# Performance work log

Measured on AMD Instinct MI355X. Metric: run time of the kernel, lower is better.

Reference implementation:

```python
import jax, jax.numpy as jnp
import numpy as np

NUM_TAG = 1024
TAG_DIM = 128
COMMITMENT_COST = 0.25
B, W = 128, 1024


def setup_inputs() -> dict:
    key = jax.random.key(0)
    k1, k2 = jax.random.split(key)
    inputs = jax.random.normal(k1, (B, W, TAG_DIM), dtype=jnp.float32)
    # torch init: uniform_(-1/num_tag, 1/num_tag)
    codebook = jax.random.uniform(k2, (NUM_TAG, TAG_DIM), dtype=jnp.float32,
                                  minval=-1.0 / NUM_TAG, maxval=1.0 / NUM_TAG)
    return {"inputs": inputs, "codebook": codebook}


def reference(inputs, codebook):
    # inputs: [B, W, D], codebook: [K, D]
    D = inputs.shape[-1]
    flat = inputs.reshape(-1, D)  # [N, D]
    distances = (jnp.sum(flat * flat, axis=1, keepdims=True)
                 + jnp.sum(codebook * codebook, axis=1)
                 - 2.0 * flat @ codebook.T)
    encoding_indices = jnp.argmin(distances, axis=1)  # [N]
    quantized = codebook[encoding_indices].reshape(inputs.shape)  # [B, W, D]
    e_latent_loss = jnp.mean((jax.lax.stop_gradient(quantized) - inputs) ** 2)
    q_latent_loss = jnp.mean((quantized - jax.lax.stop_gradient(inputs)) ** 2)
    vq_loss = q_latent_loss + COMMITMENT_COST * e_latent_loss
    # straight-through estimator
    quantized_st = inputs + jax.lax.stop_gradient(quantized - inputs)
    return (quantized_st, vq_loss, encoding_indices.reshape(inputs.shape[:-1]))
```

## Files before the change

kernel.cpp:

```cpp
#include <hip/hip_runtime.h>

#define NUM_TAG 1024
#define TAG_DIM 128
#define NROWS   131072
#define FLAG_M  1.25e-4f
#define RPG     8
#define RF      4

typedef __attribute__((ext_vector_type(8))) short short8;
typedef __attribute__((ext_vector_type(4))) float f32x4;

__device__ inline void split2(float xv, unsigned short& h, unsigned short& m) {
    unsigned xb = __float_as_uint(xv);
    unsigned hb = xb & 0xFFFF0000u;
    float r1 = xv - __uint_as_float(hb);
    unsigned mb = __float_as_uint(r1) & 0xFFFF0000u;
    h = (unsigned short)(hb >> 16);
    m = (unsigned short)(mb >> 16);
}

__device__ inline void gld_lds16(const void* g, void* l) {
    __builtin_amdgcn_global_load_lds(
        (const __attribute__((address_space(1))) void*)g,
        (__attribute__((address_space(3))) void*)l, 16, 0, 0);
}

__global__ __launch_bounds__(256) void prep_kernel(
    const float* __restrict__ cb, float* __restrict__ scc,
    unsigned short* __restrict__ cbf, int* __restrict__ count)
{
    int t = blockIdx.x * 256 + threadIdx.x;
    if (t == 0) count[0] = 0;
    {
        int l  = t & 63;
        int s  = (t >> 6) & 3;
        int ch = t >> 8;
        int k  = ch * 16 + (l & 15);
        int d0 = s * 32 + (l >> 4) * 8;
        const float4* xp = reinterpret_cast<const float4*>(cb) + k * 32 + (d0 >> 2);
        float4 v0 = xp[0], v1 = xp[1];
        float xv[8] = {v0.x, v0.y, v0.z, v0.w, v1.x, v1.y, v1.z, v1.w};
        short8 hh, mm;
#pragma unroll
        for (int e = 0; e < 8; ++e) {
            unsigned short h, m;
            split2(xv[e], h, m);
            hh[e] = (short)h; mm[e] = (short)m;
        }
        long baseh = (long)ch * 4096 + (((0 * 4) + s) * 64 + l) * 8;
        long basem = (long)ch * 4096 + (((1 * 4) + s) * 64 + l) * 8;
        *reinterpret_cast<short8*>(cbf + baseh) = hh;
        *reinterpret_cast<short8*>(cbf + basem) = mm;
    }
    if (t < NUM_TAG) {
        const float4* row = reinterpret_cast<const float4*>(cb) + t * (TAG_DIM / 4);
        float s = 0.f;
#pragma unroll
        for (int i = 0; i < TAG_DIM / 4; ++i) {
            float4 v = row[i];
            s += v.x * v.x; s += v.y * v.y; s += v.z * v.z; s += v.w * v.w;
        }
        scc[t] = s;
    }
}

__global__ __launch_bounds__(64, 2) void argmin_mfma_kernel(
    const float* __restrict__ x,
    const unsigned short* __restrict__ cbf,
    const float* __restrict__ scc,
    float* __restrict__ fidx_out,
    int* __restrict__ list, int* __restrict__ count)
{
    __shared__ __align__(16) unsigned short lds[2][4096];
    __shared__ float scc_lds[NUM_TAG];

    const int l   = threadIdx.x & 63;
    const int l15 = l & 15;
    const int l4  = l >> 4;
    const int row0 = blockIdx.x * 64;

    const float4* gsrc = reinterpret_cast<const float4*>(cbf);

#pragma unroll
    for (int i = 0; i < 4; ++i)
        gld_lds16(reinterpret_cast<const float4*>(scc) + i * 64 + l,
                  (void*)(scc_lds + (i * 64 + l) * 4));
#pragma unroll
    for (int i = 0; i < 8; ++i)
        gld_lds16(gsrc + i * 64 + l, (void*)&lds[0][(i * 64 + l) * 8]);
#pragma unroll
    for (int i = 0; i < 8; ++i)
        gld_lds16(gsrc + 512 + i * 64 + l, (void*)&lds[1][(i * 64 + l) * 8]);

    short8 Ah[RF][4], Am[RF][4];
#pragma unroll
    for (int rf = 0; rf < RF; ++rf) {
        const float4* xp = reinterpret_cast<const float4*>(x) +
                           (long)(row0 + rf * 16 + l15) * 32 + l4 * 2;
#pragma unroll
        for (int s = 0; s < 4; ++s) {
            float4 v0 = xp[s * 8];
            float4 v1 = xp[s * 8 + 1];
            float xv[8] = {v0.x, v0.y, v0.z, v0.w, v1.x, v1.y, v1.z, v1.w};
#pragma unroll
            for (int e = 0; e < 8; ++e) {
                unsigned short h, m;
                split2(xv[e], h, m);
                Ah[rf][s][e] = (short)h;
                Am[rf][s][e] = (short)m;
            }
        }
    }

    float m1[RF][4], m2[RF][4]; int i1[RF][4];
#pragma unroll
    for (int rf = 0; rf < RF; ++rf)
#pragma unroll
        for (int r = 0; r < 4; ++r) { m1[rf][r] = 3.4e38f; m2[rf][r] = 3.4e38f; i1[rf][r] = 0; }

    for (int ch = 0; ch < 64; ++ch) {
        const int b = ch & 1;
        if (ch < 63) { asm volatile("s_waitcnt vmcnt(8)" ::: "memory"); }
        else         { asm volatile("s_waitcnt vmcnt(0)" ::: "memory"); }
        __builtin_amdgcn_sched_barrier(0);

        short8 Bh[4], Bm[4];
#pragma unroll
        for (int s = 0; s < 4; ++s) {
            Bh[s] = *reinterpret_cast<const short8*>(&lds[b][(((0 * 4) + s) * 64 + l) * 8]);
            Bm[s] = *reinterpret_cast<const short8*>(&lds[b][(((1 * 4) + s) * 64 + l) * 8]);
        }
        const float sccv = scc_lds[ch * 16 + l15];

        asm volatile("s_waitcnt lgkmcnt(0)" ::: "memory");
        __builtin_amdgcn_sched_barrier(0);

        if (ch + 2 < 64) {
            const float4* gp = gsrc + (ch + 2) * 512 + l;
#pragma unroll
            for (int i = 0; i < 8; ++i)
                gld_lds16(gp + i * 64, (void*)&lds[b][(i * 64 + l) * 8]);
        }

        f32x4 acc[RF];
#pragma unroll
        for (int rf = 0; rf < RF; ++rf) acc[rf] = (f32x4)0.f;

#pragma unroll
        for (int s = 0; s < 4; ++s)
#pragma unroll
            for (int rf = 0; rf < RF; ++rf) {
                acc[rf] = __builtin_amdgcn_mfma_f32_16x16x32_bf16(Ah[rf][s], Bm[s], acc[rf], 0, 0, 0);
                acc[rf] = __builtin_amdgcn_mfma_f32_16x16x32_bf16(Am[rf][s], Bh[s], acc[rf], 0, 0, 0);
                acc[rf] = __builtin_amdgcn_mfma_f32_16x16x32_bf16(Ah[rf][s], Bh[s], acc[rf], 0, 0, 0);
            }

        const int k = ch * 16 + l15;
#pragma unroll
        for (int rf = 0; rf < RF; ++rf)
#pragma unroll
            for (int r = 0; r < 4; ++r) {
                float score = sccv - 2.0f * acc[rf][r];
                m2[rf][r] = __builtin_amdgcn_fmed3f(score, m1[rf][r], m2[rf][r]);
                i1[rf][r] = (score < m1[rf][r]) ? k : i1[rf][r];
                m1[rf][r] = fminf(m1[rf][r], score);
            }
    }

#pragma unroll
    for (int rf = 0; rf < RF; ++rf)
#pragma unroll
        for (int r = 0; r < 4; ++r) {
            float v1 = m1[rf][r], v2 = m2[rf][r]; int ii = i1[rf][r];
#pragma unroll
            for (int mk = 1; mk < 16; mk <<= 1) {
                float o1 = __shfl_xor(v1, mk, 64);
                float o2 = __shfl_xor(v2, mk, 64);
                int   oi = __shfl_xor(ii, mk, 64);
                float n2 = fminf(fminf(v2, o2), fmaxf(v1, o1));
                if (o1 < v1 || (o1 == v1 && oi < ii)) { v1 = o1; ii = oi; }
                v2 = n2;
            }
            if (l15 == 0) {
                int row = row0 + rf * 16 + l4 * 4 + r;
                fidx_out[row] = (float)ii;
                if (v2 - v1 <= FLAG_M) {
                    int pos = atomicAdd(count, 1);
                    list[pos] = row;
                }
            }
        }
}

__global__ __launch_bounds__(256) void exact_fix_kernel(
    const float* __restrict__ x, const float* __restrict__ cb,
    const float* __restrict__ scc, const int* __restrict__ list,
    const int* __restrict__ count, float* __restrict__ fidx_out)
{
    __shared__ float4 Xs[RPG][32];
    __shared__ float  sxxs[RPG];
    __shared__ float  wrv[RPG][4];
    __shared__ int    wri[RPG][4];
    __shared__ int    rows_s[RPG];

    const int tid  = threadIdx.x;
    const int lane = tid & 63;
    const int wv   = tid >> 6;
    const int nflag = count[0];
    const int ngroups = (nflag + RPG - 1) / RPG;

    for (int g = blockIdx.x; g < ngroups; g += gridDim.x) {
        const int nr = min(RPG, nflag - g * RPG);
        if (tid < RPG)
            rows_s[tid] = list[g * RPG + min(tid, nr - 1)];
        __syncthreads();
        {
            int r = tid >> 5, i = tid & 31;
            Xs[r][i] = reinterpret_cast<const float4*>(x)[(long)rows_s[r] * 32 + i];
        }
        __syncthreads();
        if (tid < RPG) {
            float s = 0.f;
            for (int i = 0; i < 32; ++i) {
                float4 v = Xs[tid][i];
                s += v.x * v.x; s += v.y * v.y; s += v.z * v.z; s += v.w * v.w;
            }
            sxxs[tid] = s;
        }
        __syncthreads();

        float acc[RPG][4];
#pragma unroll
        for (int r = 0; r < RPG; ++r)
#pragma unroll
            for (int j = 0; j < 4; ++j) acc[r][j] = 0.f;

        const float4* crow = reinterpret_cast<const float4*>(cb) + (tid * 4) * 32;
        for (int i = 0; i < 32; ++i) {
            float4 xv[RPG];
#pragma unroll
            for (int r = 0; r < RPG; ++r) xv[r] = Xs[r][i];
#pragma unroll
            for (int j = 0; j < 4; ++j) {
                float4 c = crow[j * 32 + i];
#pragma unroll
                for (int r = 0; r < RPG; ++r) {
                    acc[r][j] += xv[r].x * c.x;
                    acc[r][j] += xv[r].y * c.y;
                    acc[r][j] += xv[r].z * c.z;
                    acc[r][j] += xv[r].w * c.w;
                }
            }
        }

#pragma unroll
        for (int r = 0; r < RPG; ++r) {
            float bv = 3.4e38f; int bi = 0;
            const float sxxv = sxxs[r];
#pragma unroll
            for (int j = 0; j < 4; ++j) {
                int k = tid * 4 + j;
                float s1 = sxxv + scc[k];
                float dist = s1 - 2.0f * acc[r][j];
                if (dist < bv) { bv = dist; bi = k; }
            }
#pragma unroll
            for (int mk = 1; mk < 64; mk <<= 1) {
                float ov = __shfl_xor(bv, mk, 64);
                int   oi = __shfl_xor(bi, mk, 64);
                if (ov < bv || (ov == bv && oi < bi)) { bv = ov; bi = oi; }
            }
            if (lane == 0) { wrv[r][wv] = bv; wri[r][wv] = bi; }
        }
        __syncthreads();
        if (tid < RPG && tid < nr) {
            float bv = wrv[tid][0]; int bi = wri[tid][0];
#pragma unroll
            for (int e = 1; e < 4; ++e) {
                float v = wrv[tid][e]; int oi = wri[tid][e];
                if (v < bv || (v == bv && oi < bi)) { bv = v; bi = oi; }
            }
            fidx_out[rows_s[tid]] = (float)bi;
        }
        __syncthreads();
    }
}

__global__ __launch_bounds__(256) void quant_kernel(
    const float* __restrict__ x, const float* __restrict__ cb,
    const float* __restrict__ fidx, float* __restrict__ out,
    double* __restrict__ partial)
{
    const int N4 = NROWS * (TAG_DIM / 4);
    double s = 0.0;
    for (int i = blockIdx.x * blockDim.x + threadIdx.x; i < N4; i += gridDim.x * blockDim.x) {
        int n = i >> 5;
        int d4 = i & 31;
        int k = (int)fidx[n];
        float4 xv = reinterpret_cast<const float4*>(x)[i];
        float4 qv = reinterpret_cast<const float4*>(cb)[k * 32 + d4];
        float dx = qv.x - xv.x, dy = qv.y - xv.y, dz = qv.z - xv.z, dw = qv.w - xv.w;
        float4 o;
        o.x = xv.x + dx; o.y = xv.y + dy; o.z = xv.z + dz; o.w = xv.w + dw;
        reinterpret_cast<float4*>(out)[i] = o;
        s += (double)dx * dx; s += (double)dy * dy; s += (double)dz * dz; s += (double)dw * dw;
    }
    __shared__ double sd[256];
    sd[threadIdx.x] = s;
    __syncthreads();
    for (int off = 128; off > 0; off >>= 1) {
        if (threadIdx.x < (unsigned)off) sd[threadIdx.x] += sd[threadIdx.x + off];
        __syncthreads();
    }
    if (threadIdx.x == 0) partial[blockIdx.x] = sd[0];
}

__global__ __launch_bounds__(256) void loss_kernel(
    const double* __restrict__ partial, int n, float* __restrict__ out_loss)
{
    __shared__ double sd[256];
    double s = 0.0;
    for (int i = threadIdx.x; i < n; i += 256) s += partial[i];
    sd[threadIdx.x] = s;
    __syncthreads();
    for (int off = 128; off > 0; off >>= 1) {
        if (threadIdx.x < (unsigned)off) sd[threadIdx.x] += sd[threadIdx.x + off];
        __syncthreads();
    }
    if (threadIdx.x == 0) {
        double mean = sd[0] / (double)((long long)NROWS * TAG_DIM);
        out_loss[0] = (float)(mean + 0.25 * mean);
    }
}

extern "C" void kernel_launch(void* const* d_in, const int* in_sizes, int n_in,
                              void* d_out, int out_size, void* d_ws, size_t ws_size,
                              hipStream_t stream) {
    const float* x  = (const float*)d_in[0];
    const float* cb = (const float*)d_in[1];
    float* out      = (float*)d_out;
    float* out_loss = out + (long)NROWS * TAG_DIM;
    float* out_fidx = out_loss + 1;

    char* wsb = (char*)d_ws;
    float*          scc     = (float*)(wsb);
    unsigned short* cbf     = (unsigned short*)(wsb + 4096);
    int*            list    = (int*)(wsb + 528384);
    int*            count   = (int*)(wsb + 1052672);
    double*         partial = (double*)(wsb + 1052736);

    prep_kernel       <<<64, 256, 0, stream>>>(cb, scc, cbf, count);
    argmin_mfma_kernel<<<NROWS / 64, 64, 0, stream>>>(x, cbf, scc, out_fidx, list, count);
    exact_fix_kernel  <<<512, 256, 0, stream>>>(x, cb, scc, list, count, out_fidx);
    quant_kernel      <<<2048, 256, 0, stream>>>(x, cb, out_fidx, out, partial);
    loss_kernel       <<<1, 256, 0, stream>>>(partial, 2048, out_loss);
}
```

Baseline: 249.1 us.

## Split argmin block across two waves sharing codebook LDS staging

The argmin kernel now runs two wavefronts per block, each handling 32 rows (RF 2) instead of one wave handling 64 rows. The codebook chunk loads into LDS are split between the waves, and block barriers are added around the double-buffered LDS reads and refills. The aim is lower per-wave register pressure, higher occupancy and cooperative loading. In exchange it adds two s_barrier calls per chunk and halves MFMA reuse of each B fragment per wave.

```diff
diff --git a/kernel.cpp b/kernel.cpp
--- a/kernel.cpp
+++ b/kernel.cpp
@@ -5,7 +5,7 @@
 #define NROWS   131072
 #define FLAG_M  1.25e-4f
 #define RPG     8
-#define RF      4
+#define RF      2
 
 typedef __attribute__((ext_vector_type(8))) short short8;
 typedef __attribute__((ext_vector_type(4))) float f32x4;
@@ -64,7 +64,7 @@
     }
 }
 
-__global__ __launch_bounds__(64, 2) void argmin_mfma_kernel(
+__global__ __launch_bounds__(128, 3) void argmin_mfma_kernel(
     const float* __restrict__ x,
     const unsigned short* __restrict__ cbf,
     const float* __restrict__ scc,
@@ -74,23 +74,31 @@
     __shared__ __align__(16) unsigned short lds[2][4096];
     __shared__ float scc_lds[NUM_TAG];
 
-    const int l   = threadIdx.x & 63;
+    const int tid = threadIdx.x;
+    const int w   = tid >> 6;
+    const int l   = tid & 63;
     const int l15 = l & 15;
     const int l4  = l >> 4;
-    const int row0 = blockIdx.x * 64;
+    const int row0 = blockIdx.x * 64 + w * 32;
 
     const float4* gsrc = reinterpret_cast<const float4*>(cbf);
 
 #pragma unroll
-    for (int i = 0; i < 4; ++i)
-        gld_lds16(reinterpret_cast<const float4*>(scc) + i * 64 + l,
-                  (void*)(scc_lds + (i * 64 + l) * 4));
-#pragma unroll
-    for (int i = 0; i < 8; ++i)
-        gld_lds16(gsrc + i * 64 + l, (void*)&lds[0][(i * 64 + l) * 8]);
-#pragma unroll
-    for (int i = 0; i < 8; ++i)
-        gld_lds16(gsrc + 512 + i * 64 + l, (void*)&lds[1][(i * 64 + l) * 8]);
+    for (int i = 0; i < 2; ++i) {
+        int idx = i * 128 + w * 64 + l;
+        gld_lds16(reinterpret_cast<const float4*>(scc) + idx,
+                  (void*)(scc_lds + idx * 4));
+    }
+#pragma unroll
+    for (int i = 0; i < 4; ++i) {
+        int j = w * 4 + i;
+        gld_lds16(gsrc + j * 64 + l, (void*)&lds[0][(j * 64 + l) * 8]);
+    }
+#pragma unroll
+    for (int i = 0; i < 4; ++i) {
+        int j = w * 4 + i;
+        gld_lds16(gsrc + 512 + j * 64 + l, (void*)&lds[1][(j * 64 + l) * 8]);
+    }
 
     short8 Ah[RF][4], Am[RF][4];
 #pragma unroll
@@ -120,8 +128,9 @@
 
     for (int ch = 0; ch < 64; ++ch) {
         const int b = ch & 1;
-        if (ch < 63) { asm volatile("s_waitcnt vmcnt(8)" ::: "memory"); }
+        if (ch < 63) { asm volatile("s_waitcnt vmcnt(4)" ::: "memory"); }
         else         { asm volatile("s_waitcnt vmcnt(0)" ::: "memory"); }
+        __builtin_amdgcn_s_barrier();
         __builtin_amdgcn_sched_barrier(0);
 
         short8 Bh[4], Bm[4];
@@ -134,12 +143,15 @@
 
         asm volatile("s_waitcnt lgkmcnt(0)" ::: "memory");
         __builtin_amdgcn_sched_barrier(0);
+        __builtin_amdgcn_s_barrier();
 
         if (ch + 2 < 64) {
             const float4* gp = gsrc + (ch + 2) * 512 + l;
 #pragma unroll
-            for (int i = 0; i < 8; ++i)
-                gld_lds16(gp + i * 64, (void*)&lds[b][(i * 64 + l) * 8]);
+            for (int i = 0; i < 4; ++i) {
+                int j = w * 4 + i;
+                gld_lds16(gp + j * 64, (void*)&lds[b][(j * 64 + l) * 8]);
+            }
         }
 
         f32x4 acc[RF];
@@ -350,7 +362,7 @@
     double*         partial = (double*)(wsb + 1052736);
 
     prep_kernel       <<<64, 256, 0, stream>>>(cb, scc, cbf, count);
-    argmin_mfma_kernel<<<NROWS / 64, 64, 0, stream>>>(x, cbf, scc, out_fidx, list, count);
+    argmin_mfma_kernel<<<NROWS / 64, 128, 0, stream>>>(x, cbf, scc, out_fidx, list, count);
     exact_fix_kernel  <<<512, 256, 0, stream>>>(x, cb, scc, list, count, out_fidx);
     quant_kernel      <<<2048, 256, 0, stream>>>(x, cb, out_fidx, out, partial);
     loss_kernel       <<<1, 256, 0, stream>>>(partial, 2048, out_loss);
```

Result: no change. 248.6 us (-0.2%).

## Drop codebook low-bf16 split, read codebook from global, shrink row tile

Applied to the files above, without the earlier changes.

The codebook is now stored as a single bf16 high part, so each k-chunk needs two MFMAs per row fragment instead of three. The flagging margin is widened and the exact-fix kernel gets more blocks to absorb the extra near-ties. The LDS double-buffer fed by global_load_lds is replaced by direct register loads from global memory, with a two-stage software prefetch. Rows per block drop from 64 to 32 with a higher occupancy hint. This trades fewer MFMAs and less LDS use for more approximate scores and more rows sent to the exact fallback path, plus repeated global reads of the codebook.

```diff
diff --git a/kernel.cpp b/kernel.cpp
--- a/kernel.cpp
+++ b/kernel.cpp
@@ -3,9 +3,9 @@
 #define NUM_TAG 1024
 #define TAG_DIM 128
 #define NROWS   131072
-#define FLAG_M  1.25e-4f
+#define FLAG_M  5.5e-4f
 #define RPG     8
-#define RF      4
+#define RF      2
 
 typedef __attribute__((ext_vector_type(8))) short short8;
 typedef __attribute__((ext_vector_type(4))) float f32x4;
@@ -17,12 +17,6 @@
     unsigned mb = __float_as_uint(r1) & 0xFFFF0000u;
     h = (unsigned short)(hb >> 16);
     m = (unsigned short)(mb >> 16);
-}
-
-__device__ inline void gld_lds16(const void* g, void* l) {
-    __builtin_amdgcn_global_load_lds(
-        (const __attribute__((address_space(1))) void*)g,
-        (__attribute__((address_space(3))) void*)l, 16, 0, 0);
 }
 
 __global__ __launch_bounds__(256) void prep_kernel(
@@ -40,17 +34,11 @@
         const float4* xp = reinterpret_cast<const float4*>(cb) + k * 32 + (d0 >> 2);
         float4 v0 = xp[0], v1 = xp[1];
         float xv[8] = {v0.x, v0.y, v0.z, v0.w, v1.x, v1.y, v1.z, v1.w};
-        short8 hh, mm;
-#pragma unroll
-        for (int e = 0; e < 8; ++e) {
-            unsigned short h, m;
-            split2(xv[e], h, m);
-            hh[e] = (short)h; mm[e] = (short)m;
-        }
-        long baseh = (long)ch * 4096 + (((0 * 4) + s) * 64 + l) * 8;
-        long basem = (long)ch * 4096 + (((1 * 4) + s) * 64 + l) * 8;
-        *reinterpret_cast<short8*>(cbf + baseh) = hh;
-        *reinterpret_cast<short8*>(cbf + basem) = mm;
+        short8 hh;
+#pragma unroll
+        for (int e = 0; e < 8; ++e)
+            hh[e] = (short)(unsigned short)(__float_as_uint(xv[e]) >> 16);
+        *reinterpret_cast<short8*>(cbf + (long)ch * 2048 + ((s * 64 + l) * 8)) = hh;
     }
     if (t < NUM_TAG) {
         const float4* row = reinterpret_cast<const float4*>(cb) + t * (TAG_DIM / 4);
@@ -64,33 +52,24 @@
     }
 }
 
-__global__ __launch_bounds__(64, 2) void argmin_mfma_kernel(
+__global__ __launch_bounds__(64, 3) void argmin_mfma_kernel(
     const float* __restrict__ x,
     const unsigned short* __restrict__ cbf,
     const float* __restrict__ scc,
     float* __restrict__ fidx_out,
     int* __restrict__ list, int* __restrict__ count)
 {
-    __shared__ __align__(16) unsigned short lds[2][4096];
     __shared__ float scc_lds[NUM_TAG];
 
     const int l   = threadIdx.x & 63;
     const int l15 = l & 15;
     const int l4  = l >> 4;
-    const int row0 = blockIdx.x * 64;
-
-    const float4* gsrc = reinterpret_cast<const float4*>(cbf);
+    const int row0 = blockIdx.x * 32;
 
 #pragma unroll
     for (int i = 0; i < 4; ++i)
-        gld_lds16(reinterpret_cast<const float4*>(scc) + i * 64 + l,
-                  (void*)(scc_lds + (i * 64 + l) * 4));
-#pragma unroll
-    for (int i = 0; i < 8; ++i)
-        gld_lds16(gsrc + i * 64 + l, (void*)&lds[0][(i * 64 + l) * 8]);
-#pragma unroll
-    for (int i = 0; i < 8; ++i)
-        gld_lds16(gsrc + 512 + i * 64 + l, (void*)&lds[1][(i * 64 + l) * 8]);
+        reinterpret_cast<float4*>(scc_lds)[i * 64 + l] =
+            reinterpret_cast<const float4*>(scc)[i * 64 + l];
 
     short8 Ah[RF][4], Am[RF][4];
 #pragma unroll
@@ -118,54 +97,50 @@
 #pragma unroll
         for (int r = 0; r < 4; ++r) { m1[rf][r] = 3.4e38f; m2[rf][r] = 3.4e38f; i1[rf][r] = 0; }
 
-    for (int ch = 0; ch < 64; ++ch) {
-        const int b = ch & 1;
-        if (ch < 63) { asm volatile("s_waitcnt vmcnt(8)" ::: "memory"); }
-        else         { asm volatile("s_waitcnt vmcnt(0)" ::: "memory"); }
-        __builtin_amdgcn_sched_barrier(0);
-
-        short8 Bh[4], Bm[4];
-#pragma unroll
-        for (int s = 0; s < 4; ++s) {
-            Bh[s] = *reinterpret_cast<const short8*>(&lds[b][(((0 * 4) + s) * 64 + l) * 8]);
-            Bm[s] = *reinterpret_cast<const short8*>(&lds[b][(((1 * 4) + s) * 64 + l) * 8]);
-        }
-        const float sccv = scc_lds[ch * 16 + l15];
-
-        asm volatile("s_waitcnt lgkmcnt(0)" ::: "memory");
-        __builtin_amdgcn_sched_barrier(0);
-
-        if (ch + 2 < 64) {
-            const float4* gp = gsrc + (ch + 2) * 512 + l;
-#pragma unroll
-            for (int i = 0; i < 8; ++i)
-                gld_lds16(gp + i * 64, (void*)&lds[b][(i * 64 + l) * 8]);
-        }
-
-        f32x4 acc[RF];
-#pragma unroll
-        for (int rf = 0; rf < RF; ++rf) acc[rf] = (f32x4)0.f;
-
-#pragma unroll
-        for (int s = 0; s < 4; ++s)
-#pragma unroll
-            for (int rf = 0; rf < RF; ++rf) {
-                acc[rf] = __builtin_amdgcn_mfma_f32_16x16x32_bf16(Ah[rf][s], Bm[s], acc[rf], 0, 0, 0);
-                acc[rf] = __builtin_amdgcn_mfma_f32_16x16x32_bf16(Am[rf][s], Bh[s], acc[rf], 0, 0, 0);
-                acc[rf] = __builtin_amdgcn_mfma_f32_16x16x32_bf16(Ah[rf][s], Bh[s], acc[rf], 0, 0, 0);
-            }
-
-        const int k = ch * 16 + l15;
-#pragma unroll
-        for (int rf = 0; rf < RF; ++rf)
-#pragma unroll
-            for (int r = 0; r < 4; ++r) {
-                float score = sccv - 2.0f * acc[rf][r];
-                m2[rf][r] = __builtin_amdgcn_fmed3f(score, m1[rf][r], m2[rf][r]);
-                i1[rf][r] = (score < m1[rf][r]) ? k : i1[rf][r];
-                m1[rf][r] = fminf(m1[rf][r], score);
-            }
-    }
+    const unsigned short* gb = cbf + l * 8;
+
+#define LDB(CH, B)                                                              \
+    {                                                                           \
+        _Pragma("unroll")                                                       \
+        for (int s_ = 0; s_ < 4; ++s_)                                          \
+            B[s_] = *reinterpret_cast<const short8*>(gb + (CH) * 2048 + s_ * 512); \
+    }
+
+#define CMPFOLD(CH, B)                                                          \
+    {                                                                           \
+        const float sccv_ = scc_lds[(CH) * 16 + l15];                           \
+        f32x4 acc_[RF];                                                         \
+        _Pragma("unroll")                                                       \
+        for (int rf_ = 0; rf_ < RF; ++rf_) acc_[rf_] = (f32x4)0.f;              \
+        _Pragma("unroll")                                                       \
+        for (int s_ = 0; s_ < 4; ++s_)                                          \
+            _Pragma("unroll")                                                   \
+            for (int rf_ = 0; rf_ < RF; ++rf_) {                                \
+                acc_[rf_] = __builtin_amdgcn_mfma_f32_16x16x32_bf16(Am[rf_][s_], B[s_], acc_[rf_], 0, 0, 0); \
+                acc_[rf_] = __builtin_amdgcn_mfma_f32_16x16x32_bf16(Ah[rf_][s_], B[s_], acc_[rf_], 0, 0, 0); \
+            }                                                                   \
+        const int k_ = (CH) * 16 + l15;                                         \
+        _Pragma("unroll")                                                       \
+        for (int rf_ = 0; rf_ < RF; ++rf_)                                      \
+            _Pragma("unroll")                                                   \
+            for (int r_ = 0; r_ < 4; ++r_) {                                    \
+                float score_ = sccv_ - 2.0f * acc_[rf_][r_];                    \
+                m2[rf_][r_] = __builtin_amdgcn_fmed3f(score_, m1[rf_][r_], m2[rf_][r_]); \
+                i1[rf_][r_] = (score_ < m1[rf_][r_]) ? k_ : i1[rf_][r_];        \
+                m1[rf_][r_] = fminf(m1[rf_][r_], score_);                       \
+            }                                                                   \
+    }
+
+    short8 B0[4], B1[4];
+    LDB(0, B0);
+    for (int ch = 0; ch < 64; ch += 2) {
+        LDB(ch + 1, B1);
+        CMPFOLD(ch, B0);
+        if (ch + 2 < 64) LDB(ch + 2, B0);
+        CMPFOLD(ch + 1, B1);
+    }
+#undef LDB
+#undef CMPFOLD
 
 #pragma unroll
     for (int rf = 0; rf < RF; ++rf)
@@ -345,13 +320,13 @@
     char* wsb = (char*)d_ws;
     float*          scc     = (float*)(wsb);
     unsigned short* cbf     = (unsigned short*)(wsb + 4096);
-    int*            list    = (int*)(wsb + 528384);
-    int*            count   = (int*)(wsb + 1052672);
-    double*         partial = (double*)(wsb + 1052736);
+    int*            list    = (int*)(wsb + 266240);
+    int*            count   = (int*)(wsb + 790528);
+    double*         partial = (double*)(wsb + 790592);
 
     prep_kernel       <<<64, 256, 0, stream>>>(cb, scc, cbf, count);
-    argmin_mfma_kernel<<<NROWS / 64, 64, 0, stream>>>(x, cbf, scc, out_fidx, list, count);
-    exact_fix_kernel  <<<512, 256, 0, stream>>>(x, cb, scc, list, count, out_fidx);
+    argmin_mfma_kernel<<<NROWS / 32, 64, 0, stream>>>(x, cbf, scc, out_fidx, list, count);
+    exact_fix_kernel  <<<2048, 256, 0, stream>>>(x, cb, scc, list, count, out_fidx);
     quant_kernel      <<<2048, 256, 0, stream>>>(x, cb, out_fidx, out, partial);
     loss_kernel       <<<1, 256, 0, stream>>>(partial, 2048, out_loss);
 }
```

Measured after the change: 508.5 us. +104.1%, slower.

## Drop codebook low-half MFMA pass, widen flag margin, transpose codebook for exact fix

Applied to the files above, without the earlier changes.

The screening pass now splits only the input into bf16 high and mid parts and multiplies both by the codebook's high part. This removes one of the three MFMAs and halves the codebook staging in LDS. To compensate for the lower precision, the near-tie flag margin is widened, so more rows go to the exact fp32 fix kernel. That kernel is rewritten to read a transposed codebook with coalesced per-thread loads and to process 16 rows per group. Block size in rows, occupancy bounds and grid sizes are also retuned, and the scc LDS load becomes a plain copy.

```diff
diff --git a/kernel.cpp b/kernel.cpp
--- a/kernel.cpp
+++ b/kernel.cpp
@@ -3,9 +3,9 @@
 #define NUM_TAG 1024
 #define TAG_DIM 128
 #define NROWS   131072
-#define FLAG_M  1.25e-4f
-#define RPG     8
-#define RF      4
+#define FLAG_M  5.5e-4f
+#define RPG     16
+#define RF      2
 
 typedef __attribute__((ext_vector_type(8))) short short8;
 typedef __attribute__((ext_vector_type(4))) float f32x4;
@@ -27,7 +27,8 @@
 
 __global__ __launch_bounds__(256) void prep_kernel(
     const float* __restrict__ cb, float* __restrict__ scc,
-    unsigned short* __restrict__ cbf, int* __restrict__ count)
+    unsigned short* __restrict__ cbf, float* __restrict__ cbT,
+    int* __restrict__ count)
 {
     int t = blockIdx.x * 256 + threadIdx.x;
     if (t == 0) count[0] = 0;
@@ -40,17 +41,13 @@
         const float4* xp = reinterpret_cast<const float4*>(cb) + k * 32 + (d0 >> 2);
         float4 v0 = xp[0], v1 = xp[1];
         float xv[8] = {v0.x, v0.y, v0.z, v0.w, v1.x, v1.y, v1.z, v1.w};
-        short8 hh, mm;
+        short8 hh;
 #pragma unroll
         for (int e = 0; e < 8; ++e) {
-            unsigned short h, m;
-            split2(xv[e], h, m);
-            hh[e] = (short)h; mm[e] = (short)m;
-        }
-        long baseh = (long)ch * 4096 + (((0 * 4) + s) * 64 + l) * 8;
-        long basem = (long)ch * 4096 + (((1 * 4) + s) * 64 + l) * 8;
-        *reinterpret_cast<short8*>(cbf + baseh) = hh;
-        *reinterpret_cast<short8*>(cbf + basem) = mm;
+            hh[e] = (short)(unsigned short)(__float_as_uint(xv[e]) >> 16);
+            cbT[(d0 + e) * 1024 + k] = xv[e];
+        }
+        *reinterpret_cast<short8*>(cbf + (long)ch * 2048 + ((s * 64 + l) * 8)) = hh;
     }
     if (t < NUM_TAG) {
         const float4* row = reinterpret_cast<const float4*>(cb) + t * (TAG_DIM / 4);
@@ -64,33 +61,34 @@
     }
 }
 
-__global__ __launch_bounds__(64, 2) void argmin_mfma_kernel(
+__global__ __launch_bounds__(64, 3) void argmin_mfma_kernel(
     const float* __restrict__ x,
     const unsigned short* __restrict__ cbf,
     const float* __restrict__ scc,
     float* __restrict__ fidx_out,
     int* __restrict__ list, int* __restrict__ count)
 {
-    __shared__ __align__(16) unsigned short lds[2][4096];
+    __shared__ __align__(16) unsigned short lds[2][2048];
     __shared__ float scc_lds[NUM_TAG];
 
     const int l   = threadIdx.x & 63;
     const int l15 = l & 15;
     const int l4  = l >> 4;
-    const int row0 = blockIdx.x * 64;
+    const int row0 = blockIdx.x * 32;
 
     const float4* gsrc = reinterpret_cast<const float4*>(cbf);
 
 #pragma unroll
     for (int i = 0; i < 4; ++i)
-        gld_lds16(reinterpret_cast<const float4*>(scc) + i * 64 + l,
-                  (void*)(scc_lds + (i * 64 + l) * 4));
-#pragma unroll
-    for (int i = 0; i < 8; ++i)
         gld_lds16(gsrc + i * 64 + l, (void*)&lds[0][(i * 64 + l) * 8]);
 #pragma unroll
-    for (int i = 0; i < 8; ++i)
-        gld_lds16(gsrc + 512 + i * 64 + l, (void*)&lds[1][(i * 64 + l) * 8]);
+    for (int i = 0; i < 4; ++i)
+        gld_lds16(gsrc + 256 + i * 64 + l, (void*)&lds[1][(i * 64 + l) * 8]);
+
+#pragma unroll
+    for (int i = 0; i < 4; ++i)
+        reinterpret_cast<float4*>(scc_lds)[i * 64 + l] =
+            reinterpret_cast<const float4*>(scc)[i * 64 + l];
 
     short8 Ah[RF][4], Am[RF][4];
 #pragma unroll
@@ -120,25 +118,23 @@
 
     for (int ch = 0; ch < 64; ++ch) {
         const int b = ch & 1;
-        if (ch < 63) { asm volatile("s_waitcnt vmcnt(8)" ::: "memory"); }
+        if (ch < 63) { asm volatile("s_waitcnt vmcnt(4)" ::: "memory"); }
         else         { asm volatile("s_waitcnt vmcnt(0)" ::: "memory"); }
         __builtin_amdgcn_sched_barrier(0);
 
-        short8 Bh[4], Bm[4];
-#pragma unroll
-        for (int s = 0; s < 4; ++s) {
-            Bh[s] = *reinterpret_cast<const short8*>(&lds[b][(((0 * 4) + s) * 64 + l) * 8]);
-            Bm[s] = *reinterpret_cast<const short8*>(&lds[b][(((1 * 4) + s) * 64 + l) * 8]);
-        }
+        short8 Bh[4];
+#pragma unroll
+        for (int s = 0; s < 4; ++s)
+            Bh[s] = *reinterpret_cast<const short8*>(&lds[b][((s * 64 + l) * 8)]);
         const float sccv = scc_lds[ch * 16 + l15];
 
         asm volatile("s_waitcnt lgkmcnt(0)" ::: "memory");
         __builtin_amdgcn_sched_barrier(0);
 
         if (ch + 2 < 64) {
-            const float4* gp = gsrc + (ch + 2) * 512 + l;
-#pragma unroll
-            for (int i = 0; i < 8; ++i)
+            const float4* gp = gsrc + (ch + 2) * 256 + l;
+#pragma unroll
+            for (int i = 0; i < 4; ++i)
                 gld_lds16(gp + i * 64, (void*)&lds[b][(i * 64 + l) * 8]);
         }
 
@@ -150,7 +146,6 @@
         for (int s = 0; s < 4; ++s)
 #pragma unroll
             for (int rf = 0; rf < RF; ++rf) {
-                acc[rf] = __builtin_amdgcn_mfma_f32_16x16x32_bf16(Ah[rf][s], Bm[s], acc[rf], 0, 0, 0);
                 acc[rf] = __builtin_amdgcn_mfma_f32_16x16x32_bf16(Am[rf][s], Bh[s], acc[rf], 0, 0, 0);
                 acc[rf] = __builtin_amdgcn_mfma_f32_16x16x32_bf16(Ah[rf][s], Bh[s], acc[rf], 0, 0, 0);
             }
@@ -193,15 +188,15 @@
 }
 
 __global__ __launch_bounds__(256) void exact_fix_kernel(
-    const float* __restrict__ x, const float* __restrict__ cb,
+    const float* __restrict__ x, const float* __restrict__ cbT,
     const float* __restrict__ scc, const int* __restrict__ list,
     const int* __restrict__ count, float* __restrict__ fidx_out)
 {
-    __shared__ float4 Xs[RPG][32];
-    __shared__ float  sxxs[RPG];
-    __shared__ float  wrv[RPG][4];
-    __shared__ int    wri[RPG][4];
-    __shared__ int    rows_s[RPG];
+    __shared__ float Xs[RPG][TAG_DIM];
+    __shared__ float sxxs[RPG];
+    __shared__ float wrv[RPG][4];
+    __shared__ int   wri[RPG][4];
+    __shared__ int   rows_s[RPG];
 
     const int tid  = threadIdx.x;
     const int lane = tid & 63;
@@ -214,15 +209,16 @@
         if (tid < RPG)
             rows_s[tid] = list[g * RPG + min(tid, nr - 1)];
         __syncthreads();
-        {
-            int r = tid >> 5, i = tid & 31;
-            Xs[r][i] = reinterpret_cast<const float4*>(x)[(long)rows_s[r] * 32 + i];
+        for (int t2 = tid; t2 < RPG * 32; t2 += 256) {
+            int r = t2 >> 5, i = t2 & 31;
+            reinterpret_cast<float4*>(&Xs[r][0])[i] =
+                reinterpret_cast<const float4*>(x)[(long)rows_s[r] * 32 + i];
         }
         __syncthreads();
         if (tid < RPG) {
             float s = 0.f;
             for (int i = 0; i < 32; ++i) {
-                float4 v = Xs[tid][i];
+                float4 v = reinterpret_cast<float4*>(&Xs[tid][0])[i];
                 s += v.x * v.x; s += v.y * v.y; s += v.z * v.z; s += v.w * v.w;
             }
             sxxs[tid] = s;
@@ -235,20 +231,26 @@
 #pragma unroll
             for (int j = 0; j < 4; ++j) acc[r][j] = 0.f;
 
-        const float4* crow = reinterpret_cast<const float4*>(cb) + (tid * 4) * 32;
-        for (int i = 0; i < 32; ++i) {
-            float4 xv[RPG];
-#pragma unroll
-            for (int r = 0; r < RPG; ++r) xv[r] = Xs[r][i];
-#pragma unroll
-            for (int j = 0; j < 4; ++j) {
-                float4 c = crow[j * 32 + i];
+        for (int d4 = 0; d4 < 32; ++d4) {
+            float4 xq[RPG];
+#pragma unroll
+            for (int r = 0; r < RPG; ++r)
+                xq[r] = reinterpret_cast<float4*>(&Xs[r][0])[d4];
+#pragma unroll
+            for (int e = 0; e < 4; ++e) {
+                const int d = d4 * 4 + e;
+                float c0 = cbT[d * 1024 + 0 * 256 + tid];
+                float c1 = cbT[d * 1024 + 1 * 256 + tid];
+                float c2 = cbT[d * 1024 + 2 * 256 + tid];
+                float c3 = cbT[d * 1024 + 3 * 256 + tid];
 #pragma unroll
                 for (int r = 0; r < RPG; ++r) {
-                    acc[r][j] += xv[r].x * c.x;
-                    acc[r][j] += xv[r].y * c.y;
-                    acc[r][j] += xv[r].z * c.z;
-                    acc[r][j] += xv[r].w * c.w;
+                    float xv = (e == 0) ? xq[r].x : (e == 1) ? xq[r].y
+                             : (e == 2) ? xq[r].z : xq[r].w;
+                    acc[r][0] += xv * c0;
+                    acc[r][1] += xv * c1;
+                    acc[r][2] += xv * c2;
+                    acc[r][3] += xv * c3;
                 }
             }
         }
@@ -259,7 +261,7 @@
             const float sxxv = sxxs[r];
 #pragma unroll
             for (int j = 0; j < 4; ++j) {
-                int k = tid * 4 + j;
+                int k = j * 256 + tid;
                 float s1 = sxxv + scc[k];
                 float dist = s1 - 2.0f * acc[r][j];
                 if (dist < bv) { bv = dist; bi = k; }
@@ -345,13 +347,14 @@
     char* wsb = (char*)d_ws;
     float*          scc     = (float*)(wsb);
     unsigned short* cbf     = (unsigned short*)(wsb + 4096);
-    int*            list    = (int*)(wsb + 528384);
-    int*            count   = (int*)(wsb + 1052672);
-    double*         partial = (double*)(wsb + 1052736);
-
-    prep_kernel       <<<64, 256, 0, stream>>>(cb, scc, cbf, count);
-    argmin_mfma_kernel<<<NROWS / 64, 64, 0, stream>>>(x, cbf, scc, out_fidx, list, count);
-    exact_fix_kernel  <<<512, 256, 0, stream>>>(x, cb, scc, list, count, out_fidx);
+    float*          cbT     = (float*)(wsb + 266240);
+    int*            list    = (int*)(wsb + 790528);
+    int*            count   = (int*)(wsb + 1314816);
+    double*         partial = (double*)(wsb + 1314880);
+
+    prep_kernel       <<<64, 256, 0, stream>>>(cb, scc, cbf, cbT, count);
+    argmin_mfma_kernel<<<NROWS / 32, 64, 0, stream>>>(x, cbf, scc, out_fidx, list, count);
+    exact_fix_kernel  <<<1024, 256, 0, stream>>>(x, cbT, scc, list, count, out_fidx);
     quant_kernel      <<<2048, 256, 0, stream>>>(x, cb, out_fidx, out, partial);
     loss_kernel       <<<1, 256, 0, stream>>>(partial, 2048, out_loss);
 }
```

Result: slower. 336.2 us (+34.9%).
